# Kernel optimization log

Hardware: AMD Instinct MI355X
Metric: run time of the kernel (lower is better)

Reference implementation:

```python
import math
import jax, jax.numpy as jnp
import numpy as np

B, T, D = 4, 2048, 1024
H = 16
DK = D // H


def setup_inputs() -> dict:
    key = jax.random.key(0)
    ks = jax.random.split(key, 9)
    s = 1.0 / math.sqrt(D)
    return {
        "x": jax.random.normal(ks[0], (B, T, D), dtype=jnp.float32),
        "Wq": jax.random.normal(ks[1], (D, D), dtype=jnp.float32) * s,
        "bq": jax.random.normal(ks[2], (D,), dtype=jnp.float32) * s,
        "Wk": jax.random.normal(ks[3], (D, D), dtype=jnp.float32) * s,
        "bk": jax.random.normal(ks[4], (D,), dtype=jnp.float32) * s,
        "Wv": jax.random.normal(ks[5], (D, D), dtype=jnp.float32) * s,
        "bv": jax.random.normal(ks[6], (D,), dtype=jnp.float32) * s,
        "Wo": jax.random.normal(ks[7], (D, D), dtype=jnp.float32) * s,
        "bo": jax.random.normal(ks[8], (D,), dtype=jnp.float32) * s,
    }


def reference(x, Wq, bq, Wk, bk, Wv, bv, Wo, bo):
    Bx, Tx, C = x.shape
    # projections -> [B, H, T, d_k]
    q = (x @ Wq + bq).reshape(Bx, Tx, H, DK).transpose(0, 2, 1, 3)
    k = (x @ Wk + bk).reshape(Bx, Tx, H, DK).transpose(0, 2, 1, 3)
    v = (x @ Wv + bv).reshape(Bx, Tx, H, DK).transpose(0, 2, 1, 3)
    # scores [B, H, T, T], scaled
    scores = jnp.einsum("bhqd,bhkd->bhqk", q, k) / math.sqrt(DK)
    causal = jnp.tril(jnp.ones((Tx, Tx), dtype=bool))
    scores = jnp.where(causal[None, None, :, :], scores, -jnp.inf)
    attn = jax.nn.softmax(scores, axis=-1)  # dropout p=0.0 (eval)
    out = jnp.einsum("bhqk,bhkd->bhqd", attn, v)
    out = out.transpose(0, 2, 1, 3).reshape(Bx, Tx, C)
    return out @ Wo + bo
```

## Files before the change

### kernel.cpp

```cpp
#include <hip/hip_runtime.h>
#include <stdint.h>
#include <math.h>

typedef __attribute__((ext_vector_type(8))) __bf16 bf16x8;
typedef __attribute__((ext_vector_type(4))) __bf16 bf16x4;
typedef __attribute__((ext_vector_type(4))) float f32x4;
typedef __attribute__((ext_vector_type(4))) short short4v;

__device__ __forceinline__ void load_lds16(const void* g, void* l) {
  __builtin_amdgcn_global_load_lds((__attribute__((address_space(1))) void*)(g),
                                   (__attribute__((address_space(3))) void*)(l),
                                   16, 0, 0);
}

__device__ __forceinline__ uint32_t pack_bf2(float a, float b) {
  union { __bf16 h; uint16_t u; } x, y;
  x.h = (__bf16)a; y.h = (__bf16)b;
  return (uint32_t)x.u | ((uint32_t)y.u << 16);
}

__device__ __forceinline__ short4v mk4(uint32_t lo, uint32_t hi) {
  union { uint32_t d[2]; short4v v; } u;
  u.d[0] = lo; u.d[1] = hi;
  return u.v;
}

__device__ __forceinline__ f32x4 mfma16(short4v a, short4v b, f32x4 c) {
#if defined(__has_builtin) && __has_builtin(__builtin_amdgcn_mfma_f32_16x16x16bf16_1k)
  return __builtin_amdgcn_mfma_f32_16x16x16bf16_1k(a, b, c, 0, 0, 0);
#else
  asm volatile("v_mfma_f32_16x16x16_bf16 %0, %1, %2, %0"
               : "+v"(c) : "v"(a), "v"(b));
  return c;
#endif
}

__global__ __launch_bounds__(256)
void convert_x(const float* __restrict__ xf, __bf16* __restrict__ xb) {
  const size_t i = ((size_t)blockIdx.x * 256 + threadIdx.x) * 8;
  const float4 u0 = *(const float4*)(xf + i);
  const float4 u1 = *(const float4*)(xf + i + 4);
  bf16x8 v;
  v[0] = (__bf16)u0.x; v[1] = (__bf16)u0.y; v[2] = (__bf16)u0.z; v[3] = (__bf16)u0.w;
  v[4] = (__bf16)u1.x; v[5] = (__bf16)u1.y; v[6] = (__bf16)u1.z; v[7] = (__bf16)u1.w;
  *(bf16x8*)&xb[i] = v;
}

__global__ __launch_bounds__(256)
void prep_weights(const float* __restrict__ Wq, const float* __restrict__ Wk,
                  const float* __restrict__ Wv, const float* __restrict__ Wo,
                  const float* __restrict__ bq, const float* __restrict__ bk,
                  const float* __restrict__ bv, const float* __restrict__ bo,
                  __bf16* __restrict__ Bt1, __bf16* __restrict__ Bt2,
                  float* __restrict__ bqkv, float* __restrict__ bo_f) {
  const int m = blockIdx.z;
  const float* W = (m == 0) ? Wq : (m == 1) ? Wk : (m == 2) ? Wv : Wo;
  __bf16* Out = (m == 3) ? Bt2 : Bt1 + (size_t)m * 1024 * 1024;
  const int kt = blockIdx.x * 64, nt = blockIdx.y * 64;
  __shared__ __bf16 tile[64 * 68];
  const int t = threadIdx.x;
#pragma unroll
  for (int i = 0; i < 16; i++) {
    int e = i * 256 + t;
    int r = e >> 6, c = e & 63;
    tile[r * 68 + c] = (__bf16)W[(size_t)(kt + r) * 1024 + nt + c];
  }
  __syncthreads();
#pragma unroll
  for (int i = 0; i < 16; i++) {
    int e = i * 256 + t;
    int r = e >> 6, c = e & 63;
    Out[(size_t)(nt + r) * 1024 + kt + c] = tile[c * 68 + r];
  }
  if (blockIdx.x == 0 && blockIdx.y == 0) {
    if (m < 3) {
      const float* bsrc = (m == 0) ? bq : (m == 1) ? bk : bv;
      for (int i = t; i < 1024; i += 256) bqkv[m * 1024 + i] = bsrc[i];
    } else {
      for (int i = t; i < 1024; i += 256) bo_f[i] = bo[i];
    }
  }
}

__global__ __launch_bounds__(512)
void gemm256(const __bf16* __restrict__ A, const __bf16* __restrict__ Bt,
             const float* __restrict__ bias, void* __restrict__ Cv,
             int out_f32, int M, int N, int K) {
  __shared__ __align__(16) __bf16 As[2][256 * 64];
  __shared__ __align__(16) __bf16 Bs[2][256 * 64];
  const int t = threadIdx.x, lane = t & 63, wave = t >> 6;
  const int wm = wave >> 2, wn = wave & 3;
  const int fm = lane & 15, fq = lane >> 4;
  const int bm = blockIdx.x * 256, bn = blockIdx.y * 256;

  const int srow = t >> 3;
  const int scol = ((t & 7) ^ (srow & 7)) << 3;
  const __bf16* Ag = A + (size_t)(bm + srow) * K + scol;
  const __bf16* Bg = Bt + (size_t)(bn + srow) * K + scol;

  const int kc0 = ((fq ^ (fm & 7)) << 3);
  const int kc1 = (((4 | fq) ^ (fm & 7)) << 3);

  f32x4 acc[8][4] = {};
  const int nkt = K >> 6;

#define SA_UNIT(TT, BUF, U)                                                  \
  load_lds16(Ag + (size_t)(U) * 64 * K + (size_t)(TT) * 64,                  \
             &As[BUF][(U) * 4096 + t * 8])
#define SB_UNIT(TT, BUF, U)                                                  \
  load_lds16(Bg + (size_t)(U) * 64 * K + (size_t)(TT) * 64,                  \
             &Bs[BUF][(U) * 4096 + t * 8])

  SA_UNIT(0, 0, 0); SA_UNIT(0, 0, 1); SA_UNIT(0, 0, 2); SA_UNIT(0, 0, 3);
  SB_UNIT(0, 0, 0); SB_UNIT(0, 0, 1); SB_UNIT(0, 0, 2); SB_UNIT(0, 0, 3);
  if (nkt > 1) {
    SB_UNIT(1, 1, 0); SB_UNIT(1, 1, 1); SB_UNIT(1, 1, 2); SB_UNIT(1, 1, 3);
    asm volatile("s_waitcnt vmcnt(4)" ::: "memory");
  } else {
    asm volatile("s_waitcnt vmcnt(0)" ::: "memory");
  }
  __builtin_amdgcn_s_barrier();

  for (int j = 0; j < nkt; ++j) {
    const int c = j & 1;
    const __bf16* Ac = As[c];
    const __bf16* Bc = Bs[c];
    const int ar0 = (wm * 128 + fm) * 64;
    const int br0 = (wn * 64 + fm) * 64;
    bf16x8 afl[4], afh[4], bf0[4], bf1[4];

#pragma unroll
    for (int mi = 0; mi < 4; mi++) afl[mi] = *(const bf16x8*)&Ac[ar0 + mi * 1024 + kc0];
#pragma unroll
    for (int ni = 0; ni < 4; ni++) bf0[ni] = *(const bf16x8*)&Bc[br0 + ni * 1024 + kc0];
    if (j + 1 < nkt) { SA_UNIT(j + 1, c ^ 1, 0); SA_UNIT(j + 1, c ^ 1, 2); }
    __builtin_amdgcn_s_barrier();
    __builtin_amdgcn_s_setprio(1);
#pragma unroll
    for (int mi = 0; mi < 4; mi++)
#pragma unroll
      for (int ni = 0; ni < 4; ni++)
        acc[mi][ni] = __builtin_amdgcn_mfma_f32_16x16x32_bf16(afl[mi], bf0[ni],
                                                              acc[mi][ni], 0, 0, 0);
    __builtin_amdgcn_s_setprio(0);
    __builtin_amdgcn_s_barrier();

#pragma unroll
    for (int mi = 0; mi < 4; mi++) afl[mi] = *(const bf16x8*)&Ac[ar0 + mi * 1024 + kc1];
#pragma unroll
    for (int ni = 0; ni < 4; ni++) bf1[ni] = *(const bf16x8*)&Bc[br0 + ni * 1024 + kc1];
    if (j + 1 < nkt) { SA_UNIT(j + 1, c ^ 1, 1); SA_UNIT(j + 1, c ^ 1, 3); }
    __builtin_amdgcn_s_barrier();
    __builtin_amdgcn_s_setprio(1);
#pragma unroll
    for (int mi = 0; mi < 4; mi++)
#pragma unroll
      for (int ni = 0; ni < 4; ni++)
        acc[mi][ni] = __builtin_amdgcn_mfma_f32_16x16x32_bf16(afl[mi], bf1[ni],
                                                              acc[mi][ni], 0, 0, 0);
    __builtin_amdgcn_s_setprio(0);
    __builtin_amdgcn_s_barrier();

#pragma unroll
    for (int mi = 0; mi < 4; mi++)
      afh[mi] = *(const bf16x8*)&Ac[ar0 + (mi + 4) * 1024 + kc0];
    if (j + 2 < nkt) { SB_UNIT(j + 2, c, 0); SB_UNIT(j + 2, c, 1); }
    __builtin_amdgcn_s_barrier();
    __builtin_amdgcn_s_setprio(1);
#pragma unroll
    for (int mi = 0; mi < 4; mi++)
#pragma unroll
      for (int ni = 0; ni < 4; ni++)
        acc[mi + 4][ni] = __builtin_amdgcn_mfma_f32_16x16x32_bf16(afh[mi], bf0[ni],
                                                                  acc[mi + 4][ni], 0, 0, 0);
    __builtin_amdgcn_s_setprio(0);
    __builtin_amdgcn_s_barrier();

#pragma unroll
    for (int mi = 0; mi < 4; mi++)
      afh[mi] = *(const bf16x8*)&Ac[ar0 + (mi + 4) * 1024 + kc1];
    if (j + 2 < nkt) { SB_UNIT(j + 2, c, 2); SB_UNIT(j + 2, c, 3); }
    __builtin_amdgcn_s_barrier();
    __builtin_amdgcn_s_setprio(1);
#pragma unroll
    for (int mi = 0; mi < 4; mi++)
#pragma unroll
      for (int ni = 0; ni < 4; ni++)
        acc[mi + 4][ni] = __builtin_amdgcn_mfma_f32_16x16x32_bf16(afh[mi], bf1[ni],
                                                                  acc[mi + 4][ni], 0, 0, 0);
    __builtin_amdgcn_s_setprio(0);
    if (j + 2 < nkt) asm volatile("s_waitcnt vmcnt(4)" ::: "memory");
    else asm volatile("s_waitcnt vmcnt(0)" ::: "memory");
    __builtin_amdgcn_s_barrier();
  }
#undef SA_UNIT
#undef SB_UNIT

#pragma unroll
  for (int ni = 0; ni < 4; ni++) {
    const int col = bn + wn * 64 + ni * 16 + fm;
    const float bvv = bias[col];
#pragma unroll
    for (int mi = 0; mi < 8; mi++)
#pragma unroll
      for (int r = 0; r < 4; r++) {
        const int row = bm + wm * 128 + mi * 16 + fq * 4 + r;
        const float val = acc[mi][ni][r] + bvv;
        if (out_f32) ((float*)Cv)[(size_t)row * N + col] = val;
        else ((__bf16*)Cv)[(size_t)row * N + col] = (__bf16)val;
      }
  }
}

__global__ __launch_bounds__(256)
void transpose_v(const __bf16* __restrict__ QKV, __bf16* __restrict__ Vt) {
  const int tt = blockIdx.x;
  const int bh = blockIdx.y;
  const int b = bh >> 4, h = bh & 15;
  __shared__ __bf16 tile[64 * 68];
  const int t = threadIdx.x;
#pragma unroll
  for (int i = 0; i < 16; i++) {
    int e = i * 256 + t;
    int tok = e >> 6, dk = e & 63;
    tile[tok * 68 + dk] =
        QKV[((size_t)b * 2048 + tt * 64 + tok) * 3072 + 2048 + h * 64 + dk];
  }
  __syncthreads();
#pragma unroll
  for (int i = 0; i < 16; i++) {
    int e = i * 256 + t;
    int dk = e >> 6, tok = e & 63;
    Vt[((size_t)bh * 64 + dk) * 2048 + tt * 64 + tok] = tile[tok * 68 + dk];
  }
}

__global__ __launch_bounds__(512)
void flash_attn(const __bf16* __restrict__ QKV, const __bf16* __restrict__ Vt,
                __bf16* __restrict__ O) {
  const int y = blockIdx.y;
  const int p = (y < 4) ? y : 11 - y;
  const int qhi = 15 - p, qlo = p;
  const int bh = blockIdx.x;
  const int b = bh >> 4, h = bh & 15;
  __shared__ __align__(16) __bf16 Ks[2][64 * 64];
  __shared__ __align__(16) __bf16 Vs[2][64 * 64];
  const int t = threadIdx.x, lane = t & 63, wave = t >> 6;
  const int fm = lane & 15, fq = lane >> 4;
  const int tok0 = t >> 3;
  const int csw = ((t & 7) ^ (tok0 & 7)) << 3;
  const int swb = (fm & 7) << 4;
  const int rb0 = (((fq << 4)) ^ swb) >> 1;
  const int rb1 = ((64 + (fq << 4)) ^ swb) >> 1;
  int voff[4];
#pragma unroll
  for (int nt = 0; nt < 4; nt++)
    voff[nt] = (((((nt << 1) | (fq >> 1))) ^ (fm & 7)) << 3) | ((fq & 1) << 2);

  const size_t kbase = ((size_t)b * 2048) * 3072 + 1024 + h * 64;
  const size_t vbase = (size_t)bh * 64 * 2048;
  const int nkt = 2 * qhi + 2;
  const int qmin[2] = {qhi * 128 + wave * 16, qlo * 128 + wave * 16};
  const float SC = 0.18033688011112042f;
  const float THR_RAW = 44.3614195558365f;

  bf16x8 qf[2][2];
#pragma unroll
  for (int mi = 0; mi < 2; mi++) {
    const size_t qrow = ((size_t)b * 2048 + qmin[mi] + fm) * 3072 + h * 64;
    qf[mi][0] = *(const bf16x8*)&QKV[qrow + fq * 8];
    qf[mi][1] = *(const bf16x8*)&QKV[qrow + 32 + fq * 8];
  }

  const short4v ones4 = {(short)0x3F80, (short)0x3F80, (short)0x3F80, (short)0x3F80};

  f32x4 o_acc[2][4] = {};
  float m_i[2] = {-1e30f, -1e30f}, l_i[2] = {0.f, 0.f};

#define STAGE(KT, BUF)                                                          \
  {                                                                             \
    const int kb2 = (KT) * 64;                                                  \
    load_lds16(&QKV[kbase + (size_t)(kb2 + tok0) * 3072 + csw],                 \
               &Ks[BUF][t * 8]);                                                \
    load_lds16(&Vt[vbase + (size_t)tok0 * 2048 + kb2 + csw],                    \
               &Vs[BUF][t * 8]);                                                \
  }

  STAGE(0, 0);
  __syncthreads();
  int cur = 0;

  for (int kt = 0; kt < nkt; kt++) {
    const int kb = kt * 64;
    if (kt + 1 < nkt) STAGE(kt + 1, cur ^ 1);

    const bool act0 = (kb <= qmin[0] + 15);
    const bool act1 = (kb <= qmin[1] + 15);
    if (act0) {
      const __bf16* Kc = Ks[cur];
      const __bf16* Vc = Vs[cur];

      f32x4 s[2][4];
      __builtin_amdgcn_s_setprio(1);
#pragma unroll
      for (int nt = 0; nt < 4; nt++) {
        const bf16x8 kf0 = *(const bf16x8*)&Kc[(nt * 16 + fm) * 64 + rb0];
        const bf16x8 kf1 = *(const bf16x8*)&Kc[(nt * 16 + fm) * 64 + rb1];
        {
          f32x4 z = {};
          z = __builtin_amdgcn_mfma_f32_16x16x32_bf16(kf0, qf[0][0], z, 0, 0, 0);
          z = __builtin_amdgcn_mfma_f32_16x16x32_bf16(kf1, qf[0][1], z, 0, 0, 0);
          s[0][nt] = z;
        }
        if (act1) {
          f32x4 z = {};
          z = __builtin_amdgcn_mfma_f32_16x16x32_bf16(kf0, qf[1][0], z, 0, 0, 0);
          z = __builtin_amdgcn_mfma_f32_16x16x32_bf16(kf1, qf[1][1], z, 0, 0, 0);
          s[1][nt] = z;
        }
      }
      __builtin_amdgcn_s_setprio(0);

#pragma unroll
      for (int mi = 0; mi < 2; mi++) {
        if (mi == 1 && !act1) continue;
        if (kb + 63 > qmin[mi]) {
          const int qq = qmin[mi] + fm;
#pragma unroll
          for (int nt = 0; nt < 4; nt++) {
            const int kk = kb + nt * 16 + fq * 4;
#pragma unroll
            for (int r = 0; r < 4; r++)
              if (kk + r > qq) s[mi][nt][r] = -1e30f;
          }
        }
      }

#pragma unroll
      for (int mi = 0; mi < 2; mi++) {
        if (mi == 1 && !act1) continue;

        float a = fmaxf(fmaxf(s[mi][0][0], s[mi][0][1]),
                        fmaxf(s[mi][0][2], s[mi][0][3]));
#pragma unroll
        for (int nt = 1; nt < 4; nt++)
          a = fmaxf(a, fmaxf(fmaxf(s[mi][nt][0], s[mi][nt][1]),
                             fmaxf(s[mi][nt][2], s[mi][nt][3])));
        a = fmaxf(a, __shfl_xor(a, 16, 64));
        a = fmaxf(a, __shfl_xor(a, 32, 64));
        const float rmax = a;

        if (!__all(rmax - m_i[mi] <= THR_RAW)) {
          const float mn = fmaxf(m_i[mi], rmax);
          const float al = exp2f(SC * (m_i[mi] - mn));
          m_i[mi] = mn;
          l_i[mi] *= al;
#pragma unroll
          for (int dt = 0; dt < 4; dt++)
#pragma unroll
            for (int r = 0; r < 4; r++) o_acc[mi][dt][r] *= al;
        }

        short4v pb[4];
        const float msc = -SC * m_i[mi];
#pragma unroll
        for (int nt = 0; nt < 4; nt++) {
          const float p0 = exp2f(fmaf(s[mi][nt][0], SC, msc));
          const float p1 = exp2f(fmaf(s[mi][nt][1], SC, msc));
          const float p2 = exp2f(fmaf(s[mi][nt][2], SC, msc));
          const float p3 = exp2f(fmaf(s[mi][nt][3], SC, msc));
          pb[nt] = mk4(pack_bf2(p0, p1), pack_bf2(p2, p3));
        }

        f32x4 rs = {};
#pragma unroll
        for (int nt = 0; nt < 4; nt++) rs = mfma16(ones4, pb[nt], rs);

        __builtin_amdgcn_s_setprio(1);
#pragma unroll
        for (int dt = 0; dt < 4; dt++) {
          const int rowb = (dt * 16 + fm) * 64;
          f32x4 o = o_acc[mi][dt];
#pragma unroll
          for (int nt = 0; nt < 4; nt++) {
            const short4v vf = *(const short4v*)&Vc[rowb + voff[nt]];
            o = mfma16(vf, pb[nt], o);
          }
          o_acc[mi][dt] = o;
        }
        __builtin_amdgcn_s_setprio(0);

        l_i[mi] += rs[0];
      }
    }

    __syncthreads();
    cur ^= 1;
  }

#pragma unroll
  for (int mi = 0; mi < 2; mi++) {
    const float linv = 1.f / l_i[mi];
    const size_t orow = (size_t)b * 2048 + qmin[mi] + fm;
#pragma unroll
    for (int dt = 0; dt < 4; dt++) {
      bf16x4 w;
#pragma unroll
      for (int r = 0; r < 4; r++) w[r] = (__bf16)(o_acc[mi][dt][r] * linv);
      *(bf16x4*)&O[orow * 1024 + h * 64 + dt * 16 + fq * 4] = w;
    }
  }
#undef STAGE
}

extern "C" void kernel_launch(void* const* d_in, const int* in_sizes, int n_in,
                              void* d_out, int out_size, void* d_ws, size_t ws_size,
                              hipStream_t stream) {
  const float* x = (const float*)d_in[0];
  const float* Wq = (const float*)d_in[1];
  const float* bq = (const float*)d_in[2];
  const float* Wk = (const float*)d_in[3];
  const float* bk = (const float*)d_in[4];
  const float* Wv = (const float*)d_in[5];
  const float* bv = (const float*)d_in[6];
  const float* Wo = (const float*)d_in[7];
  const float* bo = (const float*)d_in[8];

  char* ws = (char*)d_ws;
  __bf16* Bt1 = (__bf16*)(ws);
  __bf16* Bt2 = (__bf16*)(ws + 6291456);
  float* bqkv = (float*)(ws + 8388608);
  float* bo_f = (float*)(ws + 8400896);
  __bf16* QKV = (__bf16*)(ws + 8405504);
  __bf16* Vt = (__bf16*)(ws + 58737152);
  __bf16* Xb = (__bf16*)(ws + 75514368);
  __bf16* Ow = Xb;

  hipLaunchKernelGGL(convert_x, dim3(4096), dim3(256), 0, stream, x, Xb);
  hipLaunchKernelGGL(prep_weights, dim3(16, 16, 4), dim3(256), 0, stream,
                     Wq, Wk, Wv, Wo, bq, bk, bv, bo, Bt1, Bt2, bqkv, bo_f);
  hipLaunchKernelGGL(gemm256, dim3(32, 12), dim3(512), 0, stream,
                     Xb, Bt1, bqkv, (void*)QKV, 0, 8192, 3072, 1024);
  hipLaunchKernelGGL(transpose_v, dim3(32, 64), dim3(256), 0, stream, QKV, Vt);
  hipLaunchKernelGGL(flash_attn, dim3(64, 8), dim3(512), 0, stream, QKV, Vt, Ow);
  hipLaunchKernelGGL(gemm256, dim3(32, 4), dim3(512), 0, stream,
                     Ow, Bt2, bo_f, d_out, 1, 8192, 1024, 1024);
}
```

Before: 323.5 us.

## Fuse V transpose into QKV GEMM epilogue and retile GEMM to 256x128 triple-buffered

The GEMM tile shrinks from 256x256 to 256x128, with 8 waves laid out 4x2 and 64x64 per wave. The K pipeline moves from double to triple buffering, prefetching two tiles ahead. The QKV GEMM epilogue now writes the V columns straight into the transposed Vt layout, which removes the separate transpose_v kernel launch and its extra pass over V. This doubles the number of blocks, for better occupancy on the smaller output projection. The cost is that more A re-reads are needed per output and the Vt stores are 4-element strided writes.

```diff
diff --git a/kernel.cpp b/kernel.cpp
--- a/kernel.cpp
+++ b/kernel.cpp
@@ -85,13 +85,13 @@
 __global__ __launch_bounds__(512)
 void gemm256(const __bf16* __restrict__ A, const __bf16* __restrict__ Bt,
              const float* __restrict__ bias, void* __restrict__ Cv,
-             int out_f32, int M, int N, int K) {
-  __shared__ __align__(16) __bf16 As[2][256 * 64];
-  __shared__ __align__(16) __bf16 Bs[2][256 * 64];
+             __bf16* __restrict__ Vt, int out_f32, int M, int N, int K) {
+  __shared__ __align__(16) __bf16 As[3 * 256 * 64];
+  __shared__ __align__(16) __bf16 Bs[3 * 128 * 64];
   const int t = threadIdx.x, lane = t & 63, wave = t >> 6;
-  const int wm = wave >> 2, wn = wave & 3;
+  const int wm = wave >> 1, wn = wave & 1;
   const int fm = lane & 15, fq = lane >> 4;
-  const int bm = blockIdx.x * 256, bn = blockIdx.y * 256;
+  const int bm = blockIdx.x * 256, bn = blockIdx.y * 128;
 
   const int srow = t >> 3;
   const int scol = ((t & 7) ^ (srow & 7)) << 3;
@@ -100,138 +100,103 @@
 
   const int kc0 = ((fq ^ (fm & 7)) << 3);
   const int kc1 = (((4 | fq) ^ (fm & 7)) << 3);
-
-  f32x4 acc[8][4] = {};
+  const int ar0 = (wm * 64 + fm) * 64;
+  const int br0 = (wn * 64 + fm) * 64;
+
+  f32x4 acc[4][4] = {};
   const int nkt = K >> 6;
 
-#define SA_UNIT(TT, BUF, U)                                                  \
-  load_lds16(Ag + (size_t)(U) * 64 * K + (size_t)(TT) * 64,                  \
-             &As[BUF][(U) * 4096 + t * 8])
-#define SB_UNIT(TT, BUF, U)                                                  \
-  load_lds16(Bg + (size_t)(U) * 64 * K + (size_t)(TT) * 64,                  \
-             &Bs[BUF][(U) * 4096 + t * 8])
-
-  SA_UNIT(0, 0, 0); SA_UNIT(0, 0, 1); SA_UNIT(0, 0, 2); SA_UNIT(0, 0, 3);
-  SB_UNIT(0, 0, 0); SB_UNIT(0, 0, 1); SB_UNIT(0, 0, 2); SB_UNIT(0, 0, 3);
+#define SA(TT, BUF, U)                                                     \
+  load_lds16(Ag + (size_t)(U) * 64 * K + (size_t)(TT) * 64,                \
+             &As[(BUF) * 16384 + (U) * 4096 + t * 8])
+#define SB(TT, BUF, U)                                                     \
+  load_lds16(Bg + (size_t)(U) * 64 * K + (size_t)(TT) * 64,                \
+             &Bs[(BUF) * 8192 + (U) * 4096 + t * 8])
+
+  SA(0, 0, 0); SA(0, 0, 1); SA(0, 0, 2); SA(0, 0, 3); SB(0, 0, 0); SB(0, 0, 1);
   if (nkt > 1) {
-    SB_UNIT(1, 1, 0); SB_UNIT(1, 1, 1); SB_UNIT(1, 1, 2); SB_UNIT(1, 1, 3);
-    asm volatile("s_waitcnt vmcnt(4)" ::: "memory");
+    SA(1, 1, 0); SA(1, 1, 1); SA(1, 1, 2); SA(1, 1, 3); SB(1, 1, 0); SB(1, 1, 1);
+    asm volatile("s_waitcnt vmcnt(6)" ::: "memory");
   } else {
     asm volatile("s_waitcnt vmcnt(0)" ::: "memory");
   }
   __builtin_amdgcn_s_barrier();
 
+  int c = 0, c2 = 2;
   for (int j = 0; j < nkt; ++j) {
-    const int c = j & 1;
-    const __bf16* Ac = As[c];
-    const __bf16* Bc = Bs[c];
-    const int ar0 = (wm * 128 + fm) * 64;
-    const int br0 = (wn * 64 + fm) * 64;
-    bf16x8 afl[4], afh[4], bf0[4], bf1[4];
-
-#pragma unroll
-    for (int mi = 0; mi < 4; mi++) afl[mi] = *(const bf16x8*)&Ac[ar0 + mi * 1024 + kc0];
-#pragma unroll
-    for (int ni = 0; ni < 4; ni++) bf0[ni] = *(const bf16x8*)&Bc[br0 + ni * 1024 + kc0];
-    if (j + 1 < nkt) { SA_UNIT(j + 1, c ^ 1, 0); SA_UNIT(j + 1, c ^ 1, 2); }
+    const __bf16* Ac = &As[c * 16384];
+    const __bf16* Bc = &Bs[c * 8192];
+    bf16x8 af[4], bf[4];
+
+#pragma unroll
+    for (int mi = 0; mi < 4; mi++) af[mi] = *(const bf16x8*)&Ac[ar0 + mi * 1024 + kc0];
+#pragma unroll
+    for (int ni = 0; ni < 4; ni++) bf[ni] = *(const bf16x8*)&Bc[br0 + ni * 1024 + kc0];
+    if (j + 2 < nkt) { SA(j + 2, c2, 0); SA(j + 2, c2, 1); SA(j + 2, c2, 2); }
     __builtin_amdgcn_s_barrier();
     __builtin_amdgcn_s_setprio(1);
 #pragma unroll
     for (int mi = 0; mi < 4; mi++)
 #pragma unroll
       for (int ni = 0; ni < 4; ni++)
-        acc[mi][ni] = __builtin_amdgcn_mfma_f32_16x16x32_bf16(afl[mi], bf0[ni],
+        acc[mi][ni] = __builtin_amdgcn_mfma_f32_16x16x32_bf16(af[mi], bf[ni],
                                                               acc[mi][ni], 0, 0, 0);
     __builtin_amdgcn_s_setprio(0);
     __builtin_amdgcn_s_barrier();
 
 #pragma unroll
-    for (int mi = 0; mi < 4; mi++) afl[mi] = *(const bf16x8*)&Ac[ar0 + mi * 1024 + kc1];
-#pragma unroll
-    for (int ni = 0; ni < 4; ni++) bf1[ni] = *(const bf16x8*)&Bc[br0 + ni * 1024 + kc1];
-    if (j + 1 < nkt) { SA_UNIT(j + 1, c ^ 1, 1); SA_UNIT(j + 1, c ^ 1, 3); }
+    for (int mi = 0; mi < 4; mi++) af[mi] = *(const bf16x8*)&Ac[ar0 + mi * 1024 + kc1];
+#pragma unroll
+    for (int ni = 0; ni < 4; ni++) bf[ni] = *(const bf16x8*)&Bc[br0 + ni * 1024 + kc1];
+    if (j + 2 < nkt) { SA(j + 2, c2, 3); SB(j + 2, c2, 0); SB(j + 2, c2, 1); }
     __builtin_amdgcn_s_barrier();
     __builtin_amdgcn_s_setprio(1);
 #pragma unroll
     for (int mi = 0; mi < 4; mi++)
 #pragma unroll
       for (int ni = 0; ni < 4; ni++)
-        acc[mi][ni] = __builtin_amdgcn_mfma_f32_16x16x32_bf16(afl[mi], bf1[ni],
+        acc[mi][ni] = __builtin_amdgcn_mfma_f32_16x16x32_bf16(af[mi], bf[ni],
                                                               acc[mi][ni], 0, 0, 0);
     __builtin_amdgcn_s_setprio(0);
+
+    if (j + 2 < nkt) asm volatile("s_waitcnt vmcnt(6)" ::: "memory");
+    else if (j + 1 < nkt) asm volatile("s_waitcnt vmcnt(0)" ::: "memory");
     __builtin_amdgcn_s_barrier();
 
-#pragma unroll
-    for (int mi = 0; mi < 4; mi++)
-      afh[mi] = *(const bf16x8*)&Ac[ar0 + (mi + 4) * 1024 + kc0];
-    if (j + 2 < nkt) { SB_UNIT(j + 2, c, 0); SB_UNIT(j + 2, c, 1); }
-    __builtin_amdgcn_s_barrier();
-    __builtin_amdgcn_s_setprio(1);
-#pragma unroll
-    for (int mi = 0; mi < 4; mi++)
-#pragma unroll
-      for (int ni = 0; ni < 4; ni++)
-        acc[mi + 4][ni] = __builtin_amdgcn_mfma_f32_16x16x32_bf16(afh[mi], bf0[ni],
-                                                                  acc[mi + 4][ni], 0, 0, 0);
-    __builtin_amdgcn_s_setprio(0);
-    __builtin_amdgcn_s_barrier();
-
-#pragma unroll
-    for (int mi = 0; mi < 4; mi++)
-      afh[mi] = *(const bf16x8*)&Ac[ar0 + (mi + 4) * 1024 + kc1];
-    if (j + 2 < nkt) { SB_UNIT(j + 2, c, 2); SB_UNIT(j + 2, c, 3); }
-    __builtin_amdgcn_s_barrier();
-    __builtin_amdgcn_s_setprio(1);
-#pragma unroll
-    for (int mi = 0; mi < 4; mi++)
-#pragma unroll
-      for (int ni = 0; ni < 4; ni++)
-        acc[mi + 4][ni] = __builtin_amdgcn_mfma_f32_16x16x32_bf16(afh[mi], bf1[ni],
-                                                                  acc[mi + 4][ni], 0, 0, 0);
-    __builtin_amdgcn_s_setprio(0);
-    if (j + 2 < nkt) asm volatile("s_waitcnt vmcnt(4)" ::: "memory");
-    else asm volatile("s_waitcnt vmcnt(0)" ::: "memory");
-    __builtin_amdgcn_s_barrier();
-  }
-#undef SA_UNIT
-#undef SB_UNIT
-
+    c = (c == 2) ? 0 : c + 1;
+    c2 = (c2 == 2) ? 0 : c2 + 1;
+  }
+#undef SA
+#undef SB
+
+  const bool v_mode = (Vt != nullptr) && (bn >= 2048);
 #pragma unroll
   for (int ni = 0; ni < 4; ni++) {
     const int col = bn + wn * 64 + ni * 16 + fm;
     const float bvv = bias[col];
-#pragma unroll
-    for (int mi = 0; mi < 8; mi++)
-#pragma unroll
-      for (int r = 0; r < 4; r++) {
-        const int row = bm + wm * 128 + mi * 16 + fq * 4 + r;
-        const float val = acc[mi][ni][r] + bvv;
-        if (out_f32) ((float*)Cv)[(size_t)row * N + col] = val;
-        else ((__bf16*)Cv)[(size_t)row * N + col] = (__bf16)val;
+    if (v_mode) {
+      const int vcol = col - 2048;
+      const int hh = vcol >> 6, dk = vcol & 63;
+#pragma unroll
+      for (int mi = 0; mi < 4; mi++) {
+        const int row0 = bm + wm * 64 + mi * 16 + fq * 4;
+        const int b = row0 >> 11, tok = row0 & 2047;
+        bf16x4 w;
+#pragma unroll
+        for (int r = 0; r < 4; r++) w[r] = (__bf16)(acc[mi][ni][r] + bvv);
+        *(bf16x4*)&Vt[(((size_t)b * 16 + hh) * 64 + dk) * 2048 + tok] = w;
       }
-  }
-}
-
-__global__ __launch_bounds__(256)
-void transpose_v(const __bf16* __restrict__ QKV, __bf16* __restrict__ Vt) {
-  const int tt = blockIdx.x;
-  const int bh = blockIdx.y;
-  const int b = bh >> 4, h = bh & 15;
-  __shared__ __bf16 tile[64 * 68];
-  const int t = threadIdx.x;
-#pragma unroll
-  for (int i = 0; i < 16; i++) {
-    int e = i * 256 + t;
-    int tok = e >> 6, dk = e & 63;
-    tile[tok * 68 + dk] =
-        QKV[((size_t)b * 2048 + tt * 64 + tok) * 3072 + 2048 + h * 64 + dk];
-  }
-  __syncthreads();
-#pragma unroll
-  for (int i = 0; i < 16; i++) {
-    int e = i * 256 + t;
-    int dk = e >> 6, tok = e & 63;
-    Vt[((size_t)bh * 64 + dk) * 2048 + tt * 64 + tok] = tile[tok * 68 + dk];
+    } else {
+#pragma unroll
+      for (int mi = 0; mi < 4; mi++)
+#pragma unroll
+        for (int r = 0; r < 4; r++) {
+          const int row = bm + wm * 64 + mi * 16 + fq * 4 + r;
+          const float val = acc[mi][ni][r] + bvv;
+          if (out_f32) ((float*)Cv)[(size_t)row * N + col] = val;
+          else ((__bf16*)Cv)[(size_t)row * N + col] = (__bf16)val;
+        }
+    }
   }
 }
 
@@ -439,10 +404,9 @@
   hipLaunchKernelGGL(convert_x, dim3(4096), dim3(256), 0, stream, x, Xb);
   hipLaunchKernelGGL(prep_weights, dim3(16, 16, 4), dim3(256), 0, stream,
                      Wq, Wk, Wv, Wo, bq, bk, bv, bo, Bt1, Bt2, bqkv, bo_f);
-  hipLaunchKernelGGL(gemm256, dim3(32, 12), dim3(512), 0, stream,
-                     Xb, Bt1, bqkv, (void*)QKV, 0, 8192, 3072, 1024);
-  hipLaunchKernelGGL(transpose_v, dim3(32, 64), dim3(256), 0, stream, QKV, Vt);
+  hipLaunchKernelGGL(gemm256, dim3(32, 24), dim3(512), 0, stream,
+                     Xb, Bt1, bqkv, (void*)QKV, Vt, 0, 8192, 3072, 1024);
   hipLaunchKernelGGL(flash_attn, dim3(64, 8), dim3(512), 0, stream, QKV, Vt, Ow);
-  hipLaunchKernelGGL(gemm256, dim3(32, 4), dim3(512), 0, stream,
-                     Ow, Bt2, bo_f, d_out, 1, 8192, 1024, 1024);
-}
+  hipLaunchKernelGGL(gemm256, dim3(32, 8), dim3(512), 0, stream,
+                     Ow, Bt2, bo_f, d_out, (__bf16*)nullptr, 1, 8192, 1024, 1024);
+}
```

Result: faster. 299.4 us (-7.5%).
